# Kernel tuning notes

Measured on AMD Instinct MI355X. Metric: run time of the kernel, lower is better.

Reference implementation:

```python
import jax, jax.numpy as jnp
import numpy as np

V, D, L, H, B, S = 32000, 1024, 6, 16, 4, 512
HD = D // H
DF = 4 * D
EPS = 1e-3  # keras BatchNormalization default epsilon


def setup_inputs() -> dict:
    key = jax.random.key(0)
    ks = jax.random.split(key, 12)
    s = 0.02
    return {
        "sequence": jax.random.randint(ks[0], (B, S), 0, V),
        "pes": jax.random.normal(ks[1], (S, D)) * s,
        "emb": jax.random.normal(ks[2], (V, D)) * s,
        "Wq": jax.random.normal(ks[3], (L, D, D)) * s,
        "bq": jnp.zeros((L, D)),
        "Wk": jax.random.normal(ks[4], (L, D, D)) * s,
        "bk": jnp.zeros((L, D)),
        "Wv": jax.random.normal(ks[5], (L, D, D)) * s,
        "bv": jnp.zeros((L, D)),
        "Wo": jax.random.normal(ks[6], (L, D, D)) * s,
        "bo": jnp.zeros((L, D)),
        "W1": jax.random.normal(ks[7], (L, D, DF)) * s,
        "b1": jnp.zeros((L, DF)),
        "W2": jax.random.normal(ks[8], (L, DF, D)) * s,
        "b2": jnp.zeros((L, D)),
        "g1": jnp.ones((L, D)),
        "be1": jnp.zeros((L, D)),
        "g2": jnp.ones((L, D)),
        "be2": jnp.zeros((L, D)),
    }


def _bn(x, g, b):
    # keras BatchNormalization (training-mode batch stats) over all axes but channels
    m = jnp.mean(x, axis=(0, 1))
    v = jnp.var(x, axis=(0, 1))
    return g * (x - m) * jax.lax.rsqrt(v + EPS) + b


def _forward(sequence, pes, emb, Wq, bq, Wk, bk, Wv, bv, Wo, bo,
             W1, b1, W2, b2, g1, be1, g2, be2):
    x = emb[sequence] + pes[None, :, :]            # [B,S,D]
    scale = 1.0 / np.sqrt(HD)
    for i in range(L):
        q = (x @ Wq[i] + bq[i]).reshape(B, S, H, HD)
        k = (x @ Wk[i] + bk[i]).reshape(B, S, H, HD)
        v = (x @ Wv[i] + bv[i]).reshape(B, S, H, HD)
        a = jax.nn.softmax(jnp.einsum('bqhd,bkhd->bhqk', q, k) * scale, axis=-1)
        attn = jnp.einsum('bhqk,bkhd->bqhd', a, v).reshape(B, S, D) @ Wo[i] + bo[i]
        x = _bn(x + attn, g1[i], be1[i])
        ffn = jax.nn.relu(x @ W1[i] + b1[i]) @ W2[i] + b2[i]
        x = _bn(x + ffn, g2[i], be2[i])
    return x


def reference(sequence, pes, emb, Wq, bq, Wk, bk, Wv, bv, Wo, bo,
              W1, b1, W2, b2, g1, be1, g2, be2):
    return _forward(sequence, pes, emb, Wq, bq, Wk, bk, Wv, bv, Wo, bo,
                    W1, b1, W2, b2, g1, be1, g2, be2)
```

## Files before the change

kernel.cpp:

```cpp
#include <hip/hip_runtime.h>
#include <hip/hip_bf16.h>
#include <cstdint>

typedef unsigned short u16;
typedef uint32_t u32;
typedef __bf16 bf16x8 __attribute__((ext_vector_type(8)));
typedef float f32x4 __attribute__((ext_vector_type(4)));
typedef u16 u16x4 __attribute__((ext_vector_type(4)));
typedef u16 u16x8 __attribute__((ext_vector_type(8)));

#define DD 1024
#define DFF 4096
#define NTOK 2048
#define SEQ 512

__device__ __forceinline__ float bf2f(u16 u) { return __uint_as_float(((u32)u) << 16); }
__device__ __forceinline__ u16 f2bf(float f) {
  __hip_bfloat16 h = __float2bfloat16(f);
  return *reinterpret_cast<u16*>(&h);
}
__device__ __forceinline__ void gload16(const void* g, void* l) {
  __builtin_amdgcn_global_load_lds((const __attribute__((address_space(1))) u32*)g,
                                   (__attribute__((address_space(3))) u32*)l, 16, 0, 0);
}

__global__ __launch_bounds__(256) void embed_k(const int* __restrict__ seq,
    const float* __restrict__ pes, const float* __restrict__ emb,
    float* __restrict__ x, u16* __restrict__ xb, float* __restrict__ yzero) {
  int t = blockIdx.x;
  int s = t & (SEQ - 1);
  int tok = seq[t];
  int c = threadIdx.x * 4;
  float4 e = *(const float4*)(emb + (size_t)tok * DD + c);
  float4 p = *(const float4*)(pes + (size_t)s * DD + c);
  float o0 = e.x + p.x, o1 = e.y + p.y, o2 = e.z + p.z, o3 = e.w + p.w;
  size_t i = (size_t)t * DD + c;
  *(float4*)(x + i) = make_float4(o0, o1, o2, o3);
  u16x4 ob; ob[0] = f2bf(o0); ob[1] = f2bf(o1); ob[2] = f2bf(o2); ob[3] = f2bf(o3);
  *(u16x4*)(xb + i) = ob;
  *(float4*)(yzero + i) = make_float4(0.f, 0.f, 0.f, 0.f);
}

__device__ __forceinline__ void transp_tile(const float* src, u16* dst, int R, int C,
                                            int tr, int tc, int tid) {
  __shared__ float tbuf[64 * 65];
#pragma unroll
  for (int i = 0; i < 4; ++i) {
    int f = i * 256 + tid;
    int r = f >> 4, c4 = (f & 15) * 4;
    float4 a = *(const float4*)(src + (size_t)(tr + r) * C + tc + c4);
    tbuf[r * 65 + c4 + 0] = a.x;
    tbuf[r * 65 + c4 + 1] = a.y;
    tbuf[r * 65 + c4 + 2] = a.z;
    tbuf[r * 65 + c4 + 3] = a.w;
  }
  __syncthreads();
#pragma unroll
  for (int i = 0; i < 2; ++i) {
    int g = i * 256 + tid;
    int c = g >> 3, rc = g & 7;
    u16x8 v;
#pragma unroll
    for (int j = 0; j < 8; ++j) v[j] = f2bf(tbuf[(rc * 8 + j) * 65 + c]);
    *(u16x8*)(dst + (size_t)(tc + c) * R + tr + rc * 8) = v;
  }
}

__global__ __launch_bounds__(256) void transp_sq(
    const float* __restrict__ Wq, const float* __restrict__ Wk,
    const float* __restrict__ Wv, const float* __restrict__ Wo,
    u16* __restrict__ wt) {
  int bid = blockIdx.x;
  int l = bid >> 10, z = bid & 1023;
  int m = z >> 8;
  const float* w = (m == 0) ? Wq : (m == 1) ? Wk : (m == 2) ? Wv : Wo;
  const float* src = w + (size_t)l * DD * DD;
  u16* dst = wt + (size_t)l * 12582912 + (size_t)m * DD * DD;
  int t2 = z & 255;
  transp_tile(src, dst, 1024, 1024, (t2 >> 4) * 64, (t2 & 15) * 64, threadIdx.x);
}

__global__ __launch_bounds__(256) void transp_ffn(
    const float* __restrict__ W1, const float* __restrict__ W2,
    u16* __restrict__ wt) {
  int bid = blockIdx.x;
  int l = bid >> 11, z = bid & 2047;
  u16* base = wt + (size_t)l * 12582912;
  if (z < 1024) {
    const float* src = W1 + (size_t)l * DD * DFF;
    u16* dst = base + 4 * DD * DD;
    transp_tile(src, dst, 1024, 4096, (z >> 6) * 64, (z & 63) * 64, threadIdx.x);
  } else {
    int t2 = z - 1024;
    const float* src = W2 + (size_t)l * DFF * DD;
    u16* dst = base + 4 * DD * DD + DD * DFF;
    transp_tile(src, dst, 4096, 1024, (t2 >> 4) * 64, (t2 & 15) * 64, threadIdx.x);
  }
}

#define STAGEAB(buf, kk0)                                                       \
  _Pragma("unroll")                                                             \
  for (int i_ = 0; i_ < 4; ++i_) {                                              \
    int g_ = i_ * 256 + tid;                                                    \
    int r_ = g_ >> 3, b_ = g_ & 7;                                              \
    int bs_ = b_ ^ (r_ & 7);                                                    \
    gload16(Ab + (size_t)r_ * K + (kk0) + bs_ * 8,                              \
            (char*)Als + (buf) * 16384 + g_ * 16);                              \
    gload16(Bb + (size_t)r_ * K + (kk0) + bs_ * 8,                              \
            (char*)Bls + (buf) * 16384 + g_ * 16);                              \
  }

#define FRAGS_MFMA(Ac, Bc)                                                      \
  _Pragma("unroll")                                                             \
  for (int kk = 0; kk < 2; ++kk) {                                              \
    bf16x8 av[4], bv[4];                                                        \
    _Pragma("unroll")                                                           \
    for (int m = 0; m < 4; ++m) {                                               \
      int r = wr + m * 16 + lr;                                                 \
      av[m] = *(const bf16x8*)((Ac) + r * 64 + (((kk * 4 + lg) ^ (r & 7)) * 8));\
    }                                                                           \
    _Pragma("unroll")                                                           \
    for (int n = 0; n < 4; ++n) {                                               \
      int r = wc + n * 16 + lr;                                                 \
      bv[n] = *(const bf16x8*)((Bc) + r * 64 + (((kk * 4 + lg) ^ (r & 7)) * 8));\
    }                                                                           \
    _Pragma("unroll")                                                           \
    for (int m = 0; m < 4; ++m)                                                 \
      _Pragma("unroll")                                                         \
      for (int n = 0; n < 4; ++n)                                               \
        acc[m][n] = __builtin_amdgcn_mfma_f32_16x16x32_bf16(av[m], bv[n],       \
                                                            acc[m][n], 0, 0, 0);\
  }

#define KLOOP(kb_, ke_)                                                         \
  STAGEAB(0, (kb_));                                                            \
  STAGEAB(1, (kb_) + 64);                                                       \
  {                                                                             \
    int cur = 0;                                                                \
    for (int k0 = (kb_); k0 < (ke_); k0 += 64) {                                \
      if (k0 + 64 < (ke_)) asm volatile("s_waitcnt vmcnt(8)" ::: "memory");     \
      else                 asm volatile("s_waitcnt vmcnt(0)" ::: "memory");     \
      __builtin_amdgcn_s_barrier();                                             \
      asm volatile("" ::: "memory");                                            \
      const u16* Ac = Als + cur * 8192;                                         \
      const u16* Bc = Bls + cur * 8192;                                         \
      FRAGS_MFMA(Ac, Bc);                                                       \
      __builtin_amdgcn_s_barrier();                                             \
      asm volatile("" ::: "memory");                                            \
      if (k0 + 128 < (ke_)) { STAGEAB(cur, k0 + 128); }                         \
      cur ^= 1;                                                                 \
    }                                                                           \
  }

template<int RELU, int BNL, int VT>
__global__ __launch_bounds__(256) void gemm_k(
    const u16* __restrict__ A,
    const u16* __restrict__ B0, const u16* __restrict__ B1, const u16* __restrict__ B2,
    const float* __restrict__ bi0, const float* __restrict__ bi1, const float* __restrict__ bi2,
    u16* __restrict__ outb, u16* __restrict__ vtout, int M, int N, int K) {
  int bid = blockIdx.x;
  int bn = bid & ((1 << BNL) - 1);
  int bm = (bid >> BNL) & 15;
  int z = bid >> (BNL + 4);
  const u16* Bt = (z == 0) ? B0 : (z == 1) ? B1 : B2;
  const float* bias = (z == 0) ? bi0 : (z == 1) ? bi1 : bi2;
  __shared__ __attribute__((aligned(16))) u16 Als[2 * 8192];
  __shared__ __attribute__((aligned(16))) u16 Bls[2 * 8192];
  int tid = threadIdx.x;
  int wave = tid >> 6, lane = tid & 63;
  int lr = lane & 15, lg = lane >> 4;
  int wr = (wave >> 1) * 64, wc = (wave & 1) * 64;
  int bm0 = bm * 128, bn0 = bn * 128;
  const u16* Ab = A + (size_t)bm0 * K;
  const u16* Bb = Bt + (size_t)bn0 * K;
  f32x4 acc[4][4] = {};
  KLOOP(0, K);
  size_t zoff = (size_t)z * M * N;
  float bb[4];
#pragma unroll
  for (int n = 0; n < 4; ++n) bb[n] = bias[bn0 + wc + n * 16 + lr];
#pragma unroll
  for (int m = 0; m < 4; ++m) {
    int row0 = bm0 + wr + m * 16 + lg * 4;
#pragma unroll
    for (int n = 0; n < 4; ++n) {
      int col = bn0 + wc + n * 16 + lr;
      if (VT && z == 2) {
        u16x4 ov;
#pragma unroll
        for (int j = 0; j < 4; ++j) ov[j] = f2bf(acc[m][n][j] + bb[n]);
        int b = row0 >> 9, s0 = row0 & 511;
        int h = col >> 6, hd = col & 63;
        *(u16x4*)(vtout + ((size_t)(((b << 4) + h) << 6) + hd) * 512 + s0) = ov;
      } else {
#pragma unroll
        for (int j = 0; j < 4; ++j) {
          float v = acc[m][n][j] + bb[n];
          if (RELU) v = fmaxf(v, 0.f);
          outb[zoff + (size_t)(row0 + j) * N + col] = f2bf(v);
        }
      }
    }
  }
}

__global__ __launch_bounds__(256) void gemm_splitk(
    const u16* __restrict__ A, const u16* __restrict__ Bt,
    float* __restrict__ out, int M, int N, int K, int KS) {
  int bid = blockIdx.x;
  int bn = bid & 7;
  int bm = (bid >> 3) & 15;
  int zz = bid >> 7;
  __shared__ __attribute__((aligned(16))) u16 Als[2 * 8192];
  __shared__ __attribute__((aligned(16))) u16 Bls[2 * 8192];
  int tid = threadIdx.x;
  int wave = tid >> 6, lane = tid & 63;
  int lr = lane & 15, lg = lane >> 4;
  int wr = (wave >> 1) * 64, wc = (wave & 1) * 64;
  int bm0 = bm * 128, bn0 = bn * 128;
  int kb = zz * KS, ke = kb + KS;
  const u16* Ab = A + (size_t)bm0 * K;
  const u16* Bb = Bt + (size_t)bn0 * K;
  f32x4 acc[4][4] = {};
  KLOOP(kb, ke);
#pragma unroll
  for (int m = 0; m < 4; ++m) {
    int row0 = bm0 + wr + m * 16 + lg * 4;
#pragma unroll
    for (int n = 0; n < 4; ++n) {
      int col = bn0 + wc + n * 16 + lr;
#pragma unroll
      for (int j = 0; j < 4; ++j)
        atomicAdd(out + (size_t)(row0 + j) * N + col, acc[m][n][j]);
    }
  }
}

__global__ __launch_bounds__(256) void attn_k(const u16* __restrict__ q,
    const u16* __restrict__ k, const u16* __restrict__ vt, u16* __restrict__ o) {
  int bid = blockIdx.x;
  int bh = ((bid & 7) << 3) | ((bid >> 3) & 7);
  int q0 = (bid >> 6) * 16;
  int b = bh >> 4, h = bh & 15;
  int tid = threadIdx.x;
  int wave = tid >> 6, lane = tid & 63;
  int lr = lane & 15, lg = lane >> 4;
  __shared__ __attribute__((aligned(16))) float sc[16 * 512];
  __shared__ __attribute__((aligned(16))) u16 Qs[16 * 64];
  __shared__ __attribute__((aligned(16))) u16 Ks[64 * 64];
  __shared__ __attribute__((aligned(16))) u16 Vs[64 * 64];
  __shared__ float red[16][17];
  __shared__ float rscale[16];
  if (tid < 128) {
    int r = tid >> 3, c = tid & 7;
    u16x8 t = *(const u16x8*)(q + (size_t)(b * SEQ + q0 + r) * DD + h * 64 + c * 8);
    *(u16x8*)(Qs + r * 64 + ((c ^ (r & 7)) * 8)) = t;
  }
  __syncthreads();
  bf16x8 qa[2];
#pragma unroll
  for (int kk = 0; kk < 2; ++kk)
    qa[kk] = *(const bf16x8*)(Qs + lr * 64 + (((kk * 4 + lg) ^ (lr & 7)) * 8));
  for (int kt = 0; kt < 8; ++kt) {
    const u16* kb0 = k + (size_t)(b * SEQ + kt * 64) * DD + h * 64;
#pragma unroll
    for (int i = 0; i < 2; ++i) {
      int g = i * 256 + tid;
      int r = g >> 3, c = g & 7;
      u16x8 t = *(const u16x8*)(kb0 + (size_t)r * DD + c * 8);
      *(u16x8*)(Ks + r * 64 + ((c ^ (r & 7)) * 8)) = t;
    }
    __syncthreads();
    f32x4 sacc = {};
#pragma unroll
    for (int kk = 0; kk < 2; ++kk) {
      int rr = wave * 16 + lr;
      bf16x8 kb = *(const bf16x8*)(Ks + rr * 64 + (((kk * 4 + lg) ^ (rr & 7)) * 8));
      sacc = __builtin_amdgcn_mfma_f32_16x16x32_bf16(qa[kk], kb, sacc, 0, 0, 0);
    }
#pragma unroll
    for (int j = 0; j < 4; ++j) {
      int row = lg * 4 + j;
      int col = kt * 64 + wave * 16 + lr;
      sc[row * 512 + (col ^ row)] = sacc[j] * 0.125f;
    }
    __syncthreads();
  }
  int r = tid & 15, ch = tid >> 4;
  float vr[32];
  float pmax = -3.0e38f;
#pragma unroll
  for (int i = 0; i < 32; ++i) {
    int c = ch * 32 + i;
    float xv = sc[r * 512 + (c ^ r)];
    vr[i] = xv;
    pmax = fmaxf(pmax, xv);
  }
  red[r][ch] = pmax;
  __syncthreads();
  float m = -3.0e38f;
#pragma unroll
  for (int i = 0; i < 16; ++i) m = fmaxf(m, red[r][i]);
  __syncthreads();
  float psum = 0.f;
#pragma unroll
  for (int i = 0; i < 32; ++i) {
    float e = __expf(vr[i] - m);
    vr[i] = e;
    psum += e;
  }
  red[r][ch] = psum;
  __syncthreads();
  float l = 0.f;
#pragma unroll
  for (int i = 0; i < 16; ++i) l += red[r][i];
  if (ch == 0) rscale[r] = 1.0f / l;
  u16* P = (u16*)sc;
#pragma unroll
  for (int i = 0; i < 32; ++i) {
    int c = ch * 32 + i;
    P[r * 512 + (((c >> 3) ^ (r & 7)) * 8) + (c & 7)] = f2bf(vr[i]);
  }
  f32x4 oacc = {};
  for (int kt = 0; kt < 8; ++kt) {
    __syncthreads();
    const u16* vb0 = vt + (size_t)bh * 64 * SEQ + kt * 64;
#pragma unroll
    for (int i = 0; i < 2; ++i) {
      int g = i * 256 + tid;
      int rr = g >> 3, c = g & 7;
      u16x8 t = *(const u16x8*)(vb0 + (size_t)rr * SEQ + c * 8);
      *(u16x8*)(Vs + rr * 64 + ((c ^ (rr & 7)) * 8)) = t;
    }
    __syncthreads();
#pragma unroll
    for (int kk = 0; kk < 2; ++kk) {
      int cb = kt * 8 + kk * 4 + lg;
      bf16x8 pa = *(const bf16x8*)(P + lr * 512 + ((cb ^ (lr & 7)) * 8));
      int rr = wave * 16 + lr;
      bf16x8 vb = *(const bf16x8*)(Vs + rr * 64 + (((kk * 4 + lg) ^ (rr & 7)) * 8));
      oacc = __builtin_amdgcn_mfma_f32_16x16x32_bf16(pa, vb, oacc, 0, 0, 0);
    }
  }
  __syncthreads();
  float* Of = sc;
#pragma unroll
  for (int j = 0; j < 4; ++j)
    Of[(lg * 4 + j) * 68 + wave * 16 + lr] = oacc[j] * rscale[lg * 4 + j];
  __syncthreads();
  {
    int rr = tid >> 4, c0 = (tid & 15) * 4;
    u16x4 ov;
#pragma unroll
    for (int j = 0; j < 4; ++j) ov[j] = f2bf(Of[rr * 68 + c0 + j]);
    *(u16x4*)(o + (size_t)(b * SEQ + q0 + rr) * DD + h * 64 + c0) = ov;
  }
}

__global__ __launch_bounds__(256) void bn_stats_f(const float* __restrict__ accin,
    const float* __restrict__ bias, const float* __restrict__ resid,
    float* __restrict__ part) {
  int c = blockIdx.x * 256 + threadIdx.x;
  int r0 = blockIdx.y * 32;
  float b = bias[c];
  float s = 0.f, s2 = 0.f;
  for (int r = 0; r < 32; ++r) {
    size_t idx = (size_t)(r0 + r) * DD + c;
    float v = accin[idx] + b + resid[idx];
    s += v; s2 += v * v;
  }
  size_t idx = ((size_t)blockIdx.y * DD + c) * 2;
  part[idx] = s; part[idx + 1] = s2;
}

__global__ __launch_bounds__(256) void bn_reduce_k(const float* __restrict__ part,
    const float* __restrict__ g, const float* __restrict__ be, float* __restrict__ ss) {
  int c = blockIdx.x * 256 + threadIdx.x;
  float s = 0.f, s2 = 0.f;
  for (int i = 0; i < 64; ++i) {
    s += part[((size_t)i * DD + c) * 2];
    s2 += part[((size_t)i * DD + c) * 2 + 1];
  }
  float mean = s * (1.f / 2048.f);
  float var = s2 * (1.f / 2048.f) - mean * mean;
  float rs = rsqrtf(var + 1e-3f);
  float sca = g[c] * rs;
  ss[c * 2] = sca;
  ss[c * 2 + 1] = be[c] - mean * sca;
}

__global__ __launch_bounds__(256) void bn_apply_k(float* __restrict__ y,
    const float* __restrict__ ss, const float* __restrict__ bias,
    const float* __restrict__ resid, float* __restrict__ xout, u16* __restrict__ xb) {
  size_t i = ((size_t)blockIdx.x * 256 + threadIdx.x) * 4;
  int c = (int)(i & (DD - 1));
  float4 a = *(const float4*)(y + i);
  float4 rsd = *(const float4*)(resid + i);
  float v0 = a.x + bias[c] + rsd.x;
  float v1 = a.y + bias[c + 1] + rsd.y;
  float v2 = a.z + bias[c + 2] + rsd.z;
  float v3 = a.w + bias[c + 3] + rsd.w;
  float o0 = v0 * ss[c * 2] + ss[c * 2 + 1];
  float o1 = v1 * ss[(c + 1) * 2] + ss[(c + 1) * 2 + 1];
  float o2 = v2 * ss[(c + 2) * 2] + ss[(c + 2) * 2 + 1];
  float o3 = v3 * ss[(c + 3) * 2] + ss[(c + 3) * 2 + 1];
  *(float4*)(xout + i) = make_float4(o0, o1, o2, o3);
  u16x4 ob; ob[0] = f2bf(o0); ob[1] = f2bf(o1); ob[2] = f2bf(o2); ob[3] = f2bf(o3);
  *(u16x4*)(xb + i) = ob;
  *(float4*)(y + i) = make_float4(0.f, 0.f, 0.f, 0.f);
}

extern "C" void kernel_launch(void* const* d_in, const int* in_sizes, int n_in,
                              void* d_out, int out_size, void* d_ws, size_t ws_size,
                              hipStream_t stream) {
  const int* seq = (const int*)d_in[0];
  const float* pes = (const float*)d_in[1];
  const float* emb = (const float*)d_in[2];
  const float* Wq = (const float*)d_in[3];
  const float* bq = (const float*)d_in[4];
  const float* Wk = (const float*)d_in[5];
  const float* bk = (const float*)d_in[6];
  const float* Wv = (const float*)d_in[7];
  const float* bv = (const float*)d_in[8];
  const float* Wo = (const float*)d_in[9];
  const float* bo = (const float*)d_in[10];
  const float* W1 = (const float*)d_in[11];
  const float* b1 = (const float*)d_in[12];
  const float* W2 = (const float*)d_in[13];
  const float* b2 = (const float*)d_in[14];
  const float* g1 = (const float*)d_in[15];
  const float* be1 = (const float*)d_in[16];
  const float* g2 = (const float*)d_in[17];
  const float* be2 = (const float*)d_in[18];
  (void)in_sizes; (void)n_in; (void)out_size;

  if (ws_size < (size_t)203 * 1048576) return;

  char* ws = (char*)d_ws;
  const size_t MB = 1048576;
  u16* WT = (u16*)(ws);
  float* XF = (float*)(ws + 144 * MB);
  u16* XB = (u16*)(ws + 152 * MB);
  float* YF = (float*)(ws + 156 * MB);
  u16* Qb = (u16*)(ws + 164 * MB);
  u16* VT = (u16*)(ws + 176 * MB);
  u16* AT = (u16*)(ws + 180 * MB);
  u16* HB = (u16*)(ws + 184 * MB);
  float* BP = (float*)(ws + 200 * MB);
  float* SS = (float*)(ws + 201 * MB);

  transp_sq<<<6144, 256, 0, stream>>>(Wq, Wk, Wv, Wo, WT);
  transp_ffn<<<12288, 256, 0, stream>>>(W1, W2, WT);
  embed_k<<<NTOK, 256, 0, stream>>>(seq, pes, emb, XF, XB, YF);
  for (int l = 0; l < 6; ++l) {
    u16* wl = WT + (size_t)l * 12582912;
    u16* wqT = wl;
    u16* wkT = wl + 1048576;
    u16* wvT = wl + 2097152;
    u16* woT = wl + 3145728;
    u16* w1T = wl + 4194304;
    u16* w2T = wl + 8388608;
    gemm_k<0, 3, 1><<<384, 256, 0, stream>>>(XB, wqT, wkT, wvT,
        bq + l * DD, bk + l * DD, bv + l * DD, Qb, VT, NTOK, DD, DD);
    attn_k<<<2048, 256, 0, stream>>>(Qb, Qb + (size_t)NTOK * DD, VT, AT);
    gemm_splitk<<<512, 256, 0, stream>>>(AT, woT, YF, NTOK, DD, DD, DD / 4);
    bn_stats_f<<<dim3(4, 64), 256, 0, stream>>>(YF, bo + l * DD, XF, BP);
    bn_reduce_k<<<4, 256, 0, stream>>>(BP, g1 + l * DD, be1 + l * DD, SS);
    bn_apply_k<<<NTOK, 256, 0, stream>>>(YF, SS, bo + l * DD, XF, XF, XB);
    gemm_k<1, 5, 0><<<512, 256, 0, stream>>>(XB, w1T, w1T, w1T,
        b1 + l * DFF, b1 + l * DFF, b1 + l * DFF, HB, nullptr, NTOK, DFF, DD);
    gemm_splitk<<<512, 256, 0, stream>>>(HB, w2T, YF, NTOK, DD, DFF, DFF / 4);
    bn_stats_f<<<dim3(4, 64), 256, 0, stream>>>(YF, b2 + l * DD, XF, BP);
    bn_reduce_k<<<4, 256, 0, stream>>>(BP, g2 + l * DD, be2 + l * DD, SS);
    float* xfo = (l == 5) ? (float*)d_out : XF;
    bn_apply_k<<<NTOK, 256, 0, stream>>>(YF, SS, b2 + l * DD, XF, xfo, XB);
  }
}
```

Measured before the change: 1.243 ms.

## Use 256x256-tile 512-thread GEMM kernels for the FFN projections

```diff
diff --git a/kernel.cpp b/kernel.cpp
--- a/kernel.cpp
+++ b/kernel.cpp
@@ -236,6 +236,151 @@
   }
 }
 
+#define STG_A(buf, i_, kk0) {                                                   \
+    int g_ = (i_) * 512 + tid;                                                  \
+    int r_ = g_ >> 3, b_ = g_ & 7;                                              \
+    int bs_ = b_ ^ (r_ & 7);                                                    \
+    gload16(Ab + (size_t)r_ * K + (kk0) + bs_ * 8,                              \
+            (char*)Als + (buf) * 32768 + g_ * 16); }
+#define STG_B(buf, i_, kk0) {                                                   \
+    int g_ = (i_) * 512 + tid;                                                  \
+    int r_ = g_ >> 3, b_ = g_ & 7;                                              \
+    int bs_ = b_ ^ (r_ & 7);                                                    \
+    gload16(Bb + (size_t)r_ * K + (kk0) + bs_ * 8,                              \
+            (char*)Bls + (buf) * 32768 + g_ * 16); }
+
+#define PHASE256(p) {                                                           \
+    bf16x8 av[2][2], bv[4][2];                                                  \
+    _Pragma("unroll")                                                           \
+    for (int n = 0; n < 4; ++n) {                                               \
+      int rB = wc + n * 16 + lr;                                                \
+      _Pragma("unroll")                                                         \
+      for (int kk = 0; kk < 2; ++kk)                                            \
+        bv[n][kk] = *(const bf16x8*)(Bls + cur * 16384 + rB * 64 +              \
+                                     (((kk * 4 + lg) ^ (rB & 7)) * 8));         \
+    }                                                                           \
+    _Pragma("unroll")                                                           \
+    for (int mm = 0; mm < 2; ++mm) {                                            \
+      int rA = wr + ((p) * 2 + mm) * 16 + lr;                                   \
+      _Pragma("unroll")                                                         \
+      for (int kk = 0; kk < 2; ++kk)                                            \
+        av[mm][kk] = *(const bf16x8*)(Als + cur * 16384 + rA * 64 +             \
+                                      (((kk * 4 + lg) ^ (rA & 7)) * 8));        \
+    }                                                                           \
+    __builtin_amdgcn_s_setprio(1);                                              \
+    _Pragma("unroll")                                                           \
+    for (int mm = 0; mm < 2; ++mm)                                              \
+      _Pragma("unroll")                                                         \
+      for (int n = 0; n < 4; ++n)                                               \
+        _Pragma("unroll")                                                       \
+        for (int kk = 0; kk < 2; ++kk)                                          \
+          acc[(p) * 2 + mm][n] = __builtin_amdgcn_mfma_f32_16x16x32_bf16(       \
+              av[mm][kk], bv[n][kk], acc[(p) * 2 + mm][n], 0, 0, 0);            \
+    __builtin_amdgcn_s_setprio(0); }
+
+#define KLOOP256(kb_, nt_)                                                      \
+  STG_A(0, 0, (kb_)) STG_A(0, 1, (kb_)) STG_A(0, 2, (kb_)) STG_A(0, 3, (kb_))  \
+  STG_B(0, 0, (kb_)) STG_B(0, 1, (kb_)) STG_B(0, 2, (kb_)) STG_B(0, 3, (kb_))  \
+  asm volatile("s_waitcnt vmcnt(0)" ::: "memory");                              \
+  __builtin_amdgcn_s_barrier();                                                 \
+  asm volatile("" ::: "memory");                                                \
+  {                                                                             \
+    int cur = 0;                                                                \
+    for (int kt = 0; kt < (nt_); ++kt) {                                        \
+      int nk = (kb_) + (kt + 1) * 64;                                           \
+      int hn = (kt + 1 < (nt_));                                                \
+      if (hn) { STG_A(cur ^ 1, 0, nk) STG_A(cur ^ 1, 1, nk) }                   \
+      PHASE256(0)                                                               \
+      __builtin_amdgcn_s_barrier();                                             \
+      asm volatile("" ::: "memory");                                            \
+      if (hn) { STG_A(cur ^ 1, 2, nk) STG_A(cur ^ 1, 3, nk) }                   \
+      PHASE256(1)                                                               \
+      __builtin_amdgcn_s_barrier();                                             \
+      asm volatile("" ::: "memory");                                            \
+      if (hn) { STG_B(cur ^ 1, 0, nk) STG_B(cur ^ 1, 1, nk) }                   \
+      PHASE256(2)                                                               \
+      __builtin_amdgcn_s_barrier();                                             \
+      asm volatile("" ::: "memory");                                            \
+      if (hn) { STG_B(cur ^ 1, 2, nk) STG_B(cur ^ 1, 3, nk) }                   \
+      PHASE256(3)                                                               \
+      if (hn) asm volatile("s_waitcnt vmcnt(0)" ::: "memory");                  \
+      __builtin_amdgcn_s_barrier();                                             \
+      asm volatile("" ::: "memory");                                            \
+      cur ^= 1;                                                                 \
+    }                                                                           \
+  }
+
+template<int RELU>
+__global__ __launch_bounds__(512, 2) void gemm256_k(
+    const u16* __restrict__ A, const u16* __restrict__ Bt,
+    const float* __restrict__ bias, u16* __restrict__ outb,
+    int M, int N, int K, int NBN) {
+  int bid = blockIdx.x;
+  int bn = bid % NBN, bm = bid / NBN;
+  __shared__ __attribute__((aligned(16))) u16 Als[2 * 16384];
+  __shared__ __attribute__((aligned(16))) u16 Bls[2 * 16384];
+  int tid = threadIdx.x;
+  int wave = tid >> 6, lane = tid & 63;
+  int lr = lane & 15, lg = lane >> 4;
+  int wr = (wave >> 2) * 128, wc = (wave & 3) * 64;
+  int bm0 = bm * 256, bn0 = bn * 256;
+  const u16* Ab = A + (size_t)bm0 * K;
+  const u16* Bb = Bt + (size_t)bn0 * K;
+  f32x4 acc[8][4] = {};
+  int NT = K / 64;
+  KLOOP256(0, NT);
+  float bb[4];
+#pragma unroll
+  for (int n = 0; n < 4; ++n) bb[n] = bias[bn0 + wc + n * 16 + lr];
+#pragma unroll
+  for (int m = 0; m < 8; ++m) {
+    int row0 = bm0 + wr + m * 16 + lg * 4;
+#pragma unroll
+    for (int n = 0; n < 4; ++n) {
+      int col = bn0 + wc + n * 16 + lr;
+#pragma unroll
+      for (int j = 0; j < 4; ++j) {
+        float v = acc[m][n][j] + bb[n];
+        if (RELU) v = fmaxf(v, 0.f);
+        outb[(size_t)(row0 + j) * N + col] = f2bf(v);
+      }
+    }
+  }
+}
+
+__global__ __launch_bounds__(512, 2) void gemm256_splitk(
+    const u16* __restrict__ A, const u16* __restrict__ Bt,
+    float* __restrict__ out, int M, int N, int K, int KS, int NBN, int NBM) {
+  int bid = blockIdx.x;
+  int bn = bid % NBN;
+  int bm = (bid / NBN) % NBM;
+  int zz = bid / (NBN * NBM);
+  __shared__ __attribute__((aligned(16))) u16 Als[2 * 16384];
+  __shared__ __attribute__((aligned(16))) u16 Bls[2 * 16384];
+  int tid = threadIdx.x;
+  int wave = tid >> 6, lane = tid & 63;
+  int lr = lane & 15, lg = lane >> 4;
+  int wr = (wave >> 2) * 128, wc = (wave & 3) * 64;
+  int bm0 = bm * 256, bn0 = bn * 256;
+  int kb = zz * KS;
+  const u16* Ab = A + (size_t)bm0 * K;
+  const u16* Bb = Bt + (size_t)bn0 * K;
+  f32x4 acc[8][4] = {};
+  int NT = KS / 64;
+  KLOOP256(kb, NT);
+#pragma unroll
+  for (int m = 0; m < 8; ++m) {
+    int row0 = bm0 + wr + m * 16 + lg * 4;
+#pragma unroll
+    for (int n = 0; n < 4; ++n) {
+      int col = bn0 + wc + n * 16 + lr;
+#pragma unroll
+      for (int j = 0; j < 4; ++j)
+        atomicAdd(out + (size_t)(row0 + j) * N + col, acc[m][n][j]);
+    }
+  }
+}
+
 __global__ __launch_bounds__(256) void attn_k(const u16* __restrict__ q,
     const u16* __restrict__ k, const u16* __restrict__ vt, u16* __restrict__ o) {
   int bid = blockIdx.x;
@@ -467,9 +612,10 @@
     bn_stats_f<<<dim3(4, 64), 256, 0, stream>>>(YF, bo + l * DD, XF, BP);
     bn_reduce_k<<<4, 256, 0, stream>>>(BP, g1 + l * DD, be1 + l * DD, SS);
     bn_apply_k<<<NTOK, 256, 0, stream>>>(YF, SS, bo + l * DD, XF, XF, XB);
-    gemm_k<1, 5, 0><<<512, 256, 0, stream>>>(XB, w1T, w1T, w1T,
-        b1 + l * DFF, b1 + l * DFF, b1 + l * DFF, HB, nullptr, NTOK, DFF, DD);
-    gemm_splitk<<<512, 256, 0, stream>>>(HB, w2T, YF, NTOK, DD, DFF, DFF / 4);
+    gemm256_k<1><<<128, 512, 0, stream>>>(XB, w1T, b1 + l * DFF, HB,
+                                          NTOK, DFF, DD, 16);
+    gemm256_splitk<<<128, 512, 0, stream>>>(HB, w2T, YF, NTOK, DD, DFF,
+                                            1024, 4, 8);
     bn_stats_f<<<dim3(4, 64), 256, 0, stream>>>(YF, b2 + l * DD, XF, BP);
     bn_reduce_k<<<4, 256, 0, stream>>>(BP, g2 + l * DD, be2 + l * DD, SS);
     float* xfo = (l == 5) ? (float*)d_out : XF;
```

New measurement: 1.627 ms. +30.8%, slower.
